# Optimization experiments

Measured on AMD Instinct MI355X. Metric: run time of the kernel, lower is better.

## Reference

```python
import jax, jax.numpy as jnp
import numpy as np
from jax.scipy.special import logsumexp, gammaln

B, T, D, K = 2048, 512, 64, 16  # num_sequences, max_length, data_dim (tones), hidden_dim per factor


def setup_inputs() -> dict:
    key = jax.random.key(0)
    k0, k1, k2, k3, k4 = jax.random.split(key, 5)
    sequences = jax.random.randint(k0, (B, T, D), 0, 2).astype(jnp.int32)  # binary piano-roll obs
    lengths = jax.random.randint(k1, (B,), 1, T + 1).astype(jnp.int32)
    probs_w = jax.nn.softmax(jax.random.normal(k2, (K, K), dtype=jnp.float32), axis=-1)  # row-stochastic
    probs_x = jax.nn.softmax(jax.random.normal(k3, (K, K), dtype=jnp.float32), axis=-1)
    probs_y = jax.random.uniform(k4, (K, K, D), dtype=jnp.float32) * 0.98 + 0.01  # in (0.01, 0.99)
    return {"sequences": sequences, "lengths": lengths,
            "probs_w": probs_w, "probs_x": probs_x, "probs_y": probs_y}


def _dirichlet_logpdf_rows(p, conc):
    # sum over rows of Dirichlet(conc_row).log_prob(p_row)
    return (((conc - 1.0) * jnp.log(p)).sum()
            + gammaln(conc.sum(-1)).sum() - gammaln(conc).sum())


def _log_joint(sequences, lengths, probs_w, probs_x, probs_y):
    dt = probs_y.dtype
    logTw = jnp.log(probs_w)            # (K, K) transition for w factor
    logTx = jnp.log(probs_x)            # (K, K) transition for x factor
    lp = jnp.log(probs_y)               # (K, K, D)
    l1p = jnp.log1p(-probs_y)           # (K, K, D)
    Wemit = (lp - l1p).reshape(K * K, D)        # Bernoulli log-odds per joint state
    base = l1p.sum(-1).reshape(K * K)           # sum_d log(1-p)

    ys = jnp.swapaxes(sequences, 0, 1)          # (T, B, D) int
    mask = jnp.arange(T)[:, None] < lengths[None, :]  # (T, B)

    # alpha[b, w, x]: forward log-prob; initial deterministic state (w, x) = (0, 0)
    alpha0 = jnp.full((B, K, K), -1e9, dtype=dt).at[:, 0, 0].set(0.0)

    def step(alpha, inp):
        y_t, m_t = inp
        y_f = y_t.astype(dt)                                    # (B, D)
        logE = (y_f @ Wemit.T + base).reshape(B, K, K)          # emission log-prob per (w', x')
        # marginalize previous w: (B, x, w')
        tmp = logsumexp(alpha[:, :, :, None] + logTw[None, :, None, :], axis=1)
        # marginalize previous x: (B, w', x')
        new = logsumexp(tmp[:, :, :, None] + logTx[None, :, None, :], axis=1)
        new = new + logE
        alpha = jnp.where(m_t[:, None, None], new, alpha)       # frozen past sequence end
        return alpha, None

    alpha, _ = jax.lax.scan(step, alpha0, (ys, mask))
    seq_ll = logsumexp(alpha.reshape(B, K * K), axis=-1)        # (B,) marginal log-likelihood

    # priors: Dirichlet(0.9*I + 0.1) on transition rows, Beta(0.1, 0.9) on probs_y
    conc = 0.9 * jnp.eye(K, dtype=dt) + 0.1
    prior = _dirichlet_logpdf_rows(probs_w, conc) + _dirichlet_logpdf_rows(probs_x, conc)
    a, b = 0.1, 0.9
    log_beta_norm = gammaln(a) + gammaln(b) - gammaln(a + b)
    prior = prior + ((a - 1.0) * lp + (b - 1.0) * l1p).sum() - log_beta_norm * (K * K * D)

    return seq_ll.sum() + prior


def reference(sequences, lengths, probs_w, probs_x, probs_y):
    return _log_joint(sequences, lengths, probs_w, probs_x, probs_y)
```

## Files before the change

### kernel.cpp

```cpp
#include <hip/hip_runtime.h>
#include <math.h>

#define NB 2048
#define NT 512
#define ND 64

typedef float    f32x4 __attribute__((ext_vector_type(4)));
typedef short    s16x8 __attribute__((ext_vector_type(8)));

#define MFMA32(A,B,C) __builtin_amdgcn_mfma_f32_16x16x32_bf16((A),(B),(C),0,0,0)

#if __has_builtin(__builtin_amdgcn_exp2f)
#define EXP2F(x) __builtin_amdgcn_exp2f(x)
#else
#define EXP2F(x) __expf((x) * 0.6931471805599453f)
#endif
#if __has_builtin(__builtin_amdgcn_logf)
#define LOG2F(x) __builtin_amdgcn_logf(x)
#else
#define LOG2F(x) (__logf(x) * 1.4426950408889634f)
#endif
#if __has_builtin(__builtin_amdgcn_rcpf)
#define RCPF(x) __builtin_amdgcn_rcpf(x)
#else
#define RCPF(x) __fdividef(1.0f, (x))
#endif

__device__ __forceinline__ unsigned short bf16rn(float f) {
  unsigned u = __float_as_uint(f);
  unsigned r = u + 0x7FFFu + ((u >> 16) & 1u);
  return (unsigned short)(r >> 16);
}
__device__ __forceinline__ unsigned pack2(float a, float b) {
  return (unsigned)bf16rn(a) | ((unsigned)bf16rn(b) << 16);
}
__device__ __forceinline__ unsigned pack2t(float a, float b) {
  return (__float_as_uint(a) >> 16) | (__float_as_uint(b) & 0xFFFF0000u);
}

union frag8 { s16x8 s8; unsigned u[4]; };

__device__ __forceinline__ s16x8 pack8t(f32x4 x) {
  frag8 r;
  r.u[0] = pack2t(x[0], x[1]);
  r.u[1] = pack2t(x[2], x[3]);
  r.u[2] = 0u; r.u[3] = 0u;
  return r.s8;
}

__global__ void fhmm_init_sort(const float* __restrict__ py,
                               const int* __restrict__ lengths,
                               unsigned short* __restrict__ ws16,
                               float* __restrict__ partials,
                               int* __restrict__ perm)
{
  const float LOG2E = 1.4426950408889634f;
  if (blockIdx.x == 12) {
    __shared__ int hist[512];
    __shared__ int cnt[512];
    __shared__ int sa[512], sb2[512];
    const int tid = threadIdx.x;
    hist[tid] = 0; hist[tid + 256] = 0;
    cnt[tid] = 0;  cnt[tid + 256] = 0;
    __syncthreads();
    int myb[8];
#pragma unroll
    for (int u = 0; u < 8; ++u) {
      int i = tid + 256 * u;
      myb[u] = 512 - lengths[i];
      atomicAdd(&hist[myb[u]], 1);
    }
    __syncthreads();
    sa[tid] = hist[tid]; sa[tid + 256] = hist[tid + 256];
    __syncthreads();
    int* src = sa; int* dst = sb2;
    for (int off = 1; off < 512; off <<= 1) {
      for (int k = tid; k < 512; k += 256)
        dst[k] = src[k] + ((k >= off) ? src[k - off] : 0);
      __syncthreads();
      int* tp = src; src = dst; dst = tp;
    }
#pragma unroll
    for (int u = 0; u < 8; ++u) {
      int i = tid + 256 * u;
      int b2 = myb[u];
      int pos = src[b2] - hist[b2] + atomicAdd(&cnt[b2], 1);
      perm[pos] = i;
    }
    return;
  }
  int t = blockIdx.x * 256 + threadIdx.x;
  if (t < 2048) partials[t] = 0.f;
  if (t < 2048) {
    int st = t >> 7, kk = (t >> 6) & 1, l = t & 63;
    int rho = st * 16 + (l & 15);
    int s = (4 * (rho >> 6) + (rho & 3)) * 16 + ((rho >> 2) & 15);
    int d0 = kk * 32 + 8 * (l >> 4);
    unsigned short* dst = ws16 + (size_t)t * 8;
#pragma unroll
    for (int i = 0; i < 8; ++i) {
      float p = py[s * 64 + d0 + i];
      dst[i] = bf16rn((logf(p) - log1pf(-p)) * LOG2E);
    }
  } else if (t < 3072) {
    int t2 = t - 2048;
    int st = t2 >> 6, l = t2 & 63;
    unsigned short v[8] = {0, 0, 0, 0, 0, 0, 0, 0};
    if (l < 16) {
      int rho = st * 16 + l;
      int s = (4 * (rho >> 6) + (rho & 3)) * 16 + ((rho >> 2) & 15);
      float base = 0.f;
      for (int d = 0; d < 64; ++d) base += log1pf(-py[s * 64 + d]);
      base *= LOG2E;
      unsigned short hi = bf16rn(base);
      float basehi = __uint_as_float(((unsigned)hi) << 16);
      v[0] = hi;
      v[1] = bf16rn(base - basehi);
    }
    unsigned short* dst = ws16 + (size_t)(2048 + t2) * 8;
#pragma unroll
    for (int i = 0; i < 8; ++i) dst[i] = v[i];
  }
}

__global__ __launch_bounds__(256, 2) void fhmm_fwd2(
    const int* __restrict__ seq, const int* __restrict__ lengths,
    const float* __restrict__ pw, const float* __restrict__ px,
    const void* __restrict__ wfrag, const int* __restrict__ perm,
    float* __restrict__ partials)
{
  __shared__ f32x4 e_lds[4][1024];

  const int tid = threadIdx.x;
  const int wv = tid >> 6, j = tid & 63;
  const int q = j >> 4, tl = j & 15;
  const int bid = blockIdx.x;
  const int lb  = (bid < 256) ? bid : (767 - bid);
  const int b = perm[(lb << 2) | wv];
  if (b < 0 || b >= NB) return;
  f32x4* e_w = e_lds[wv];
  const s16x8* wf_g = (const s16x8*)wfrag;
  const s16x8* w2_g = wf_g + 2048;

  s16x8 twb8, txb8;
  {
    frag8 a, c;
    a.u[0] = pack2(pw[(4 * q + 0) * 16 + tl], pw[(4 * q + 1) * 16 + tl]);
    a.u[1] = pack2(pw[(4 * q + 2) * 16 + tl], pw[(4 * q + 3) * 16 + tl]);
    a.u[2] = 0u; a.u[3] = 0u;
    c.u[0] = pack2(px[(4 * q + 0) * 16 + tl], px[(4 * q + 1) * 16 + tl]);
    c.u[1] = pack2(px[(4 * q + 2) * 16 + tl], px[(4 * q + 3) * 16 + tl]);
    c.u[2] = 0u; c.u[3] = 0u;
    twb8 = a.s8; txb8 = c.s8;
  }

  s16x8 f2 = {0, 0, 0, 0, 0, 0, 0, 0};
  if (q == 0) { f2[0] = (short)0x3F80; f2[1] = (short)0x3F80; }

  s16x8 ones8;
  {
    frag8 o;
    o.u[0] = 0x3F803F80u; o.u[1] = 0x3F803F80u;
    o.u[2] = 0x3F803F80u; o.u[3] = 0x3F803F80u;
    ones8 = o.s8;
  }

  f32x4 p = {0.f, 0.f, 0.f, 0.f};
  if (j == 0) p[0] = 1.f;

  const int len = lengths[b];
  const int* ybase = seq + (size_t)b * NT * ND;

  int4 ya0, ya1, yb0, yb1;
  {
    const int* yr = ybase + (size_t)tl * ND + 8 * q;
    const int4* pp  = (const int4*)yr;
    const int4* pp2 = (const int4*)(yr + 32);
    ya0 = pp[0]; ya1 = pp[1]; yb0 = pp2[0]; yb1 = pp2[1];
  }

  float L2 = 0.f, Ls = 0.f, R = 0.f;
  const f32x4 z4 = {0.f, 0.f, 0.f, 0.f};

  for (int t0 = 0; t0 < len; t0 += 16) {
    union { s16x8 s; unsigned u[4]; } f0u, f1u;
    f0u.u[0] = (ya0.x ? 0x3F80u : 0u) | (ya0.y ? 0x3F800000u : 0u);
    f0u.u[1] = (ya0.z ? 0x3F80u : 0u) | (ya0.w ? 0x3F800000u : 0u);
    f0u.u[2] = (ya1.x ? 0x3F80u : 0u) | (ya1.y ? 0x3F800000u : 0u);
    f0u.u[3] = (ya1.z ? 0x3F80u : 0u) | (ya1.w ? 0x3F800000u : 0u);
    f1u.u[0] = (yb0.x ? 0x3F80u : 0u) | (yb0.y ? 0x3F800000u : 0u);
    f1u.u[1] = (yb0.z ? 0x3F80u : 0u) | (yb0.w ? 0x3F800000u : 0u);
    f1u.u[2] = (yb1.x ? 0x3F80u : 0u) | (yb1.y ? 0x3F800000u : 0u);
    f1u.u[3] = (yb1.z ? 0x3F80u : 0u) | (yb1.w ? 0x3F800000u : 0u);
    const s16x8 f0 = f0u.s, f1 = f1u.s;

    if (t0 + 16 < len) {
      const int* yr = ybase + (size_t)(t0 + 16 + tl) * ND + 8 * q;
      const int4* pp  = (const int4*)yr;
      const int4* pp2 = (const int4*)(yr + 32);
      ya0 = pp[0]; ya1 = pp[1]; yb0 = pp2[0]; yb1 = pp2[1];
    }

#pragma unroll
    for (int st = 0; st < 16; ++st) {
      f32x4 acc = MFMA32(w2_g[st * 64 + j], f2, z4);
      acc = MFMA32(wf_g[(2 * st + 0) * 64 + j], f0, acc);
      acc = MFMA32(wf_g[(2 * st + 1) * 64 + j], f1, acc);
      f32x4 G;
      G[0] = EXP2F(fminf(acc[0] - R, 80.f));
      G[1] = EXP2F(fminf(acc[1] - R, 80.f));
      G[2] = EXP2F(fminf(acc[2] - R, 80.f));
      G[3] = EXP2F(fminf(acc[3] - R, 80.f));
      e_w[tl * 64 + ((st * 4 + q) ^ tl)] = G;
    }

    const int nsteps = (len - t0 < 16) ? (len - t0) : 16;
    float LsC = 0.f;
    f32x4 gv = e_w[j];
    for (int it = 0; it < nsteps; ++it) {
      const f32x4 g = gv;
      const int itn = (it + 1) & 15;
      gv = e_w[itn * 64 + (j ^ itn)];
      s16x8 vb = pack8t(p);
      f32x4 P  = MFMA32(vb, twb8, z4);
      f32x4 S1 = MFMA32(vb, ones8, z4);
      f32x4 U  = MFMA32(pack8t(P), txb8, z4);
      f32x4 S2 = MFMA32(pack8t(S1), ones8, z4);
      const float s   = fmaxf(S2[0], 1e-30f);
      const float inv = RCPF(s);
      LsC += LOG2F(s);
      f32x4 pn;
      pn[0] = (U[0] * inv) * g[0];
      pn[1] = (U[1] * inv) * g[1];
      pn[2] = (U[2] * inv) * g[2];
      pn[3] = (U[3] * inv) * g[3];
      p = pn;
    }
    L2 += (float)nsteps * R;
    Ls += LsC;
    R  += LsC * 0.0625f;
  }
  {
    f32x4 F1 = MFMA32(pack8t(p), ones8, z4);
    f32x4 F2 = MFMA32(pack8t(F1), ones8, z4);
    float sf = fmaxf(F2[0], 1e-35f);
    float L = (L2 + Ls + LOG2F(sf)) * 0.6931471805599453f;
    if (j == 0) partials[b] = L;
  }
}

__global__ __launch_bounds__(256, 3) void fhmm_fwd1(
    const int* __restrict__ seq, const int* __restrict__ lengths,
    const float* __restrict__ pw, const float* __restrict__ px,
    const float* __restrict__ py, float* __restrict__ partials,
    float* __restrict__ out)
{
  const int b = blockIdx.x, tid = threadIdx.x;
  const int wp = tid >> 4, xc = tid & 15;
  float Twc[16], Txc[16], W[64], base = 0.f;
#pragma unroll
  for (int w = 0; w < 16; ++w) Twc[w] = pw[w * 16 + wp];
#pragma unroll
  for (int x = 0; x < 16; ++x) Txc[x] = px[x * 16 + xc];
#pragma unroll
  for (int d = 0; d < 64; ++d) {
    float pv = py[tid * 64 + d];
    W[d] = logf(pv) - log1pf(-pv);
    base += log1pf(-pv);
  }
  __shared__ __align__(16) float yf[64];
  __shared__ __align__(16) float v_s[256];
  __shared__ __align__(16) float tmp_s[256];
  __shared__ float red[8];
  const int len = lengths[b];
  const int* yb = seq + (size_t)b * (NT * ND);
  v_s[tid] = (tid == 0) ? 1.f : 0.f;
  float L = 0.f, ynext = 0.f;
  if (tid < 64) ynext = (float)yb[tid];
  for (int t = 0; t < len; ++t) {
    if (tid < 64) yf[tid] = ynext;
    __syncthreads();
    if (tid < 64 && (t + 1) < len) ynext = (float)yb[(t + 1) * ND + tid];
    float e0 = base, e1 = 0.f, e2 = 0.f, e3 = 0.f;
    const float4* y4p = (const float4*)yf;
#pragma unroll
    for (int i = 0; i < 16; ++i) {
      float4 y4 = y4p[i];
      e0 = fmaf(y4.x, W[4 * i + 0], e0); e1 = fmaf(y4.y, W[4 * i + 1], e1);
      e2 = fmaf(y4.z, W[4 * i + 2], e2); e3 = fmaf(y4.w, W[4 * i + 3], e3);
    }
    float e = (e0 + e1) + (e2 + e3);
    float s1a = 0.f, s1b = 0.f;
#pragma unroll
    for (int w = 0; w < 16; w += 2) {
      s1a = fmaf(Twc[w], v_s[w * 16 + xc], s1a);
      s1b = fmaf(Twc[w + 1], v_s[(w + 1) * 16 + xc], s1b);
    }
    tmp_s[tid] = s1a + s1b;
    float mm = e;
#pragma unroll
    for (int off = 32; off; off >>= 1) mm = fmaxf(mm, __shfl_xor(mm, off));
    if ((tid & 63) == 0) red[tid >> 6] = mm;
    __syncthreads();
    mm = fmaxf(fmaxf(red[0], red[1]), fmaxf(red[2], red[3]));
    float q0 = 0.f, q1 = 0.f;
    const float4* t4p = (const float4*)(tmp_s + wp * 16);
#pragma unroll
    for (int i = 0; i < 4; ++i) {
      float4 t4 = t4p[i];
      q0 = fmaf(t4.x, Txc[4 * i + 0], q0); q1 = fmaf(t4.y, Txc[4 * i + 1], q1);
      q0 = fmaf(t4.z, Txc[4 * i + 2], q0); q1 = fmaf(t4.w, Txc[4 * i + 3], q1);
    }
    float val = (q0 + q1) * __expf(e - mm);
    float s = val;
#pragma unroll
    for (int off = 32; off; off >>= 1) s += __shfl_xor(s, off);
    if ((tid & 63) == 0) red[4 + (tid >> 6)] = s;
    __syncthreads();
    s = (red[4] + red[5]) + (red[6] + red[7]);
    L += __logf(s) + mm;
    v_s[tid] = val * (1.0f / s);
  }
  if (partials) { if (tid == 0) partials[b] = L; }
  else { if (tid == 0) atomicAdd(out, L); }
}

__global__ void fhmm_finalize(const float* __restrict__ partials,
                              const float* __restrict__ pw,
                              const float* __restrict__ px,
                              const float* __restrict__ py,
                              float* __restrict__ out)
{
  const int tid = threadIdx.x;
  float a = 0.f;
  if (partials) {
#pragma unroll
    for (int i = 0; i < 8; ++i) a += partials[tid + 256 * i];
  }
  {
    int i = tid >> 4, j = tid & 15;
    if (i != j) a += -0.9f * (logf(pw[tid]) + logf(px[tid]));
  }
  for (int k = 0; k < 64; ++k) {
    float p = py[tid * 64 + k];
    a += -0.9f * logf(p) - 0.1f * log1pf(-p);
  }
  __shared__ float red[256];
  red[tid] = a;
  __syncthreads();
  for (int s = 128; s > 0; s >>= 1) {
    if (tid < s) red[tid] += red[tid + s];
    __syncthreads();
  }
  if (tid == 0) {
    const float cst =
        2.f * (16.f * 0.2846828704729192f - 240.f * 2.2527126517342055f)
        - (2.2527126517342055f + 0.0663762397347443f) * 16384.f;
    out[0] = red[0] + cst;
  }
}

extern "C" void kernel_launch(void* const* d_in, const int* in_sizes, int n_in,
                              void* d_out, int out_size, void* d_ws, size_t ws_size,
                              hipStream_t stream) {
  const int*   seq = (const int*)d_in[0];
  const int*   len = (const int*)d_in[1];
  const float* pw  = (const float*)d_in[2];
  const float* px  = (const float*)d_in[3];
  const float* py  = (const float*)d_in[4];
  float*       out = (float*)d_out;

  const size_t NEED = 65536;
  if (ws_size >= NEED) {
    unsigned short* wf = (unsigned short*)d_ws;
    float* partials = (float*)((char*)d_ws + 49152);
    int*   perm     = (int*)((char*)d_ws + 57344);
    fhmm_init_sort<<<13, 256, 0, stream>>>(py, len, wf, partials, perm);
    fhmm_fwd2<<<512, 256, 0, stream>>>(seq, len, pw, px, (const void*)wf, perm, partials);
    fhmm_finalize<<<1, 256, 0, stream>>>(partials, pw, px, py, out);
  } else if (ws_size >= 2048 * sizeof(float)) {
    float* partials = (float*)d_ws;
    fhmm_fwd1<<<NB, 256, 0, stream>>>(seq, len, pw, px, py, partials, out);
    fhmm_finalize<<<1, 256, 0, stream>>>(partials, pw, px, py, out);
  } else {
    fhmm_finalize<<<1, 256, 0, stream>>>(nullptr, pw, px, py, out);
    fhmm_fwd1<<<NB, 256, 0, stream>>>(seq, len, pw, px, py, nullptr, out);
  }
}
```

Measured before the change: 200.8 us.

## Split each sequence into parallel forward and backward halves meeting at midpoint

Adds a new kernel in which each sequence is handled by two waves: one runs the scaled forward recursion over the first half and the other runs a backward recursion from the end down to the midpoint. A separate combine kernel takes the dot product of the alpha and beta vectors to recover each sequence's log-likelihood. The aim is to halve the serial dependency chain per sequence and double the number of active waves, with emission values stored in LDS as bf16 to cut shared-memory use. The cost is an extra kernel launch, global traffic for the intermediate vectors, a larger workspace requirement, and lower precision in the stored emissions.

```diff
diff --git a/kernel.cpp b/kernel.cpp
--- a/kernel.cpp
+++ b/kernel.cpp
@@ -123,6 +123,196 @@
   }
 }
 
+__global__ __launch_bounds__(256, 4) void fhmm_fwd3(
+    const int* __restrict__ seq, const int* __restrict__ lengths,
+    const float* __restrict__ pw, const float* __restrict__ px,
+    const void* __restrict__ wfrag, const int* __restrict__ perm,
+    float* __restrict__ alphaM, float* __restrict__ betaM,
+    float* __restrict__ scal)
+{
+  __shared__ uint2 e_lds[4][1024];
+
+  const int tid = threadIdx.x;
+  const int wv = tid >> 6, j = tid & 63;
+  const int q = j >> 4, tl = j & 15;
+  const int bid = blockIdx.x;
+  const int lb  = (bid < 512) ? bid : (1535 - bid);
+  const int rank = 2 * lb + (wv >> 1);
+  const int h = wv & 1;
+  const int b = perm[rank];
+  if (b < 0 || b >= NB) return;
+  uint2* e_w = e_lds[wv];
+  const s16x8* wf_g = (const s16x8*)wfrag;
+  const s16x8* w2_g = wf_g + 2048;
+
+  s16x8 twb8, txb8;
+  {
+    frag8 a, c;
+    if (h == 0) {
+      a.u[0] = pack2(pw[(4 * q + 0) * 16 + tl], pw[(4 * q + 1) * 16 + tl]);
+      a.u[1] = pack2(pw[(4 * q + 2) * 16 + tl], pw[(4 * q + 3) * 16 + tl]);
+      c.u[0] = pack2(px[(4 * q + 0) * 16 + tl], px[(4 * q + 1) * 16 + tl]);
+      c.u[1] = pack2(px[(4 * q + 2) * 16 + tl], px[(4 * q + 3) * 16 + tl]);
+    } else {
+      a.u[0] = pack2(pw[tl * 16 + 4 * q + 0], pw[tl * 16 + 4 * q + 1]);
+      a.u[1] = pack2(pw[tl * 16 + 4 * q + 2], pw[tl * 16 + 4 * q + 3]);
+      c.u[0] = pack2(px[tl * 16 + 4 * q + 0], px[tl * 16 + 4 * q + 1]);
+      c.u[1] = pack2(px[tl * 16 + 4 * q + 2], px[tl * 16 + 4 * q + 3]);
+    }
+    a.u[2] = 0u; a.u[3] = 0u; c.u[2] = 0u; c.u[3] = 0u;
+    twb8 = a.s8; txb8 = c.s8;
+  }
+
+  s16x8 f2 = {0, 0, 0, 0, 0, 0, 0, 0};
+  if (q == 0) { f2[0] = (short)0x3F80; f2[1] = (short)0x3F80; }
+
+  s16x8 ones8;
+  {
+    frag8 o;
+    o.u[0] = 0x3F803F80u; o.u[1] = 0x3F803F80u;
+    o.u[2] = 0x3F803F80u; o.u[3] = 0x3F803F80u;
+    ones8 = o.s8;
+  }
+
+  const int len = lengths[b];
+  const int mid = len >> 1;
+  const int* ybase = seq + (size_t)b * NT * ND;
+  const f32x4 z4 = {0.f, 0.f, 0.f, 0.f};
+
+  f32x4 p;
+  if (h == 0) { p = z4; if (j == 0) p[0] = 1.f; }
+  else { p[0] = 1.f; p[1] = 1.f; p[2] = 1.f; p[3] = 1.f; }
+
+  float L2 = 0.f, Ls = 0.f, R = 0.f;
+
+  for (int k = 0;; ++k) {
+    int t_lo, ns;
+    if (h == 0) {
+      t_lo = 16 * k;
+      if (t_lo >= mid) break;
+      ns = mid - t_lo; if (ns > 16) ns = 16;
+    } else {
+      int t_hi = len - 16 * k;
+      if (t_hi <= mid) break;
+      t_lo = t_hi - 16; if (t_lo < mid) t_lo = mid;
+      ns = t_hi - t_lo;
+    }
+
+    s16x8 f0, f1;
+    {
+      int row = t_lo + tl;
+      if (row > len - 1) row = len - 1;
+      const int* yr = ybase + (size_t)row * ND + 8 * q;
+      const int4 ya0 = ((const int4*)yr)[0];
+      const int4 ya1 = ((const int4*)yr)[1];
+      const int4 yb0 = ((const int4*)(yr + 32))[0];
+      const int4 yb1 = ((const int4*)(yr + 32))[1];
+      frag8 f0u, f1u;
+      f0u.u[0] = (ya0.x ? 0x3F80u : 0u) | (ya0.y ? 0x3F800000u : 0u);
+      f0u.u[1] = (ya0.z ? 0x3F80u : 0u) | (ya0.w ? 0x3F800000u : 0u);
+      f0u.u[2] = (ya1.x ? 0x3F80u : 0u) | (ya1.y ? 0x3F800000u : 0u);
+      f0u.u[3] = (ya1.z ? 0x3F80u : 0u) | (ya1.w ? 0x3F800000u : 0u);
+      f1u.u[0] = (yb0.x ? 0x3F80u : 0u) | (yb0.y ? 0x3F800000u : 0u);
+      f1u.u[1] = (yb0.z ? 0x3F80u : 0u) | (yb0.w ? 0x3F800000u : 0u);
+      f1u.u[2] = (yb1.x ? 0x3F80u : 0u) | (yb1.y ? 0x3F800000u : 0u);
+      f1u.u[3] = (yb1.z ? 0x3F80u : 0u) | (yb1.w ? 0x3F800000u : 0u);
+      f0 = f0u.s8; f1 = f1u.s8;
+    }
+
+#pragma unroll
+    for (int st = 0; st < 16; ++st) {
+      f32x4 acc = MFMA32(w2_g[st * 64 + j], f2, z4);
+      acc = MFMA32(wf_g[(2 * st + 0) * 64 + j], f0, acc);
+      acc = MFMA32(wf_g[(2 * st + 1) * 64 + j], f1, acc);
+      float G0 = EXP2F(fminf(acc[0] - R, 80.f));
+      float G1 = EXP2F(fminf(acc[1] - R, 80.f));
+      float G2 = EXP2F(fminf(acc[2] - R, 80.f));
+      float G3 = EXP2F(fminf(acc[3] - R, 80.f));
+      e_w[tl * 64 + ((st * 4 + q) ^ tl)] = make_uint2(pack2t(G0, G1), pack2t(G2, G3));
+    }
+
+    float LsC = 0.f;
+    if (h == 0) {
+      uint2 ev = e_w[j];
+      for (int it = 0; it < ns; ++it) {
+        const uint2 ec = ev;
+        const int itn = (it + 1) & 15;
+        ev = e_w[itn * 64 + (j ^ itn)];
+        f32x4 g;
+        g[0] = __uint_as_float(ec.x << 16);
+        g[1] = __uint_as_float(ec.x & 0xFFFF0000u);
+        g[2] = __uint_as_float(ec.y << 16);
+        g[3] = __uint_as_float(ec.y & 0xFFFF0000u);
+        s16x8 vb = pack8t(p);
+        f32x4 P  = MFMA32(vb, twb8, z4);
+        f32x4 S1 = MFMA32(vb, ones8, z4);
+        f32x4 U  = MFMA32(pack8t(P), txb8, z4);
+        f32x4 S2 = MFMA32(pack8t(S1), ones8, z4);
+        const float s   = fmaxf(S2[0], 1e-30f);
+        const float inv = RCPF(s);
+        LsC += LOG2F(s);
+        p[0] = (U[0] * inv) * g[0];
+        p[1] = (U[1] * inv) * g[1];
+        p[2] = (U[2] * inv) * g[2];
+        p[3] = (U[3] * inv) * g[3];
+      }
+    } else {
+      int it0 = ns - 1;
+      uint2 ev = e_w[it0 * 64 + (j ^ it0)];
+      for (int it = it0; it >= 0; --it) {
+        const uint2 ec = ev;
+        const int itn = (it - 1) & 15;
+        ev = e_w[itn * 64 + (j ^ itn)];
+        f32x4 u4;
+        u4[0] = p[0] * __uint_as_float(ec.x << 16);
+        u4[1] = p[1] * __uint_as_float(ec.x & 0xFFFF0000u);
+        u4[2] = p[2] * __uint_as_float(ec.y << 16);
+        u4[3] = p[3] * __uint_as_float(ec.y & 0xFFFF0000u);
+        s16x8 vb = pack8t(u4);
+        f32x4 P  = MFMA32(vb, twb8, z4);
+        f32x4 S1 = MFMA32(vb, ones8, z4);
+        f32x4 U  = MFMA32(pack8t(P), txb8, z4);
+        f32x4 S2 = MFMA32(pack8t(S1), ones8, z4);
+        const float s   = fmaxf(S2[0], 1e-30f);
+        const float inv = RCPF(s);
+        LsC += LOG2F(s);
+        p[0] = U[0] * inv;
+        p[1] = U[1] * inv;
+        p[2] = U[2] * inv;
+        p[3] = U[3] * inv;
+      }
+    }
+    L2 += (float)ns * R;
+    Ls += LsC;
+    R  += LsC * 0.0625f;
+  }
+
+  {
+    float* outv = (h ? betaM : alphaM) + (size_t)b * 256 + j * 4;
+    *(f32x4*)outv = p;
+    if (j == 0) scal[2 * b + h] = L2 + Ls;
+  }
+}
+
+__global__ void fhmm_combine(const float* __restrict__ alphaM,
+                             const float* __restrict__ betaM,
+                             const float* __restrict__ scal,
+                             float* __restrict__ partials)
+{
+  const int b = blockIdx.x, tid = threadIdx.x;
+  float v = alphaM[(size_t)b * 256 + tid] * betaM[(size_t)b * 256 + tid];
+#pragma unroll
+  for (int off = 1; off < 64; off <<= 1) v += __shfl_xor(v, off);
+  __shared__ float red[4];
+  if ((tid & 63) == 0) red[tid >> 6] = v;
+  __syncthreads();
+  if (tid == 0) {
+    float dot = fmaxf((red[0] + red[1]) + (red[2] + red[3]), 1e-35f);
+    partials[b] = (scal[2 * b] + scal[2 * b + 1] + LOG2F(dot))
+                  * 0.6931471805599453f;
+  }
+}
+
 __global__ __launch_bounds__(256, 2) void fhmm_fwd2(
     const int* __restrict__ seq, const int* __restrict__ lengths,
     const float* __restrict__ pw, const float* __restrict__ px,
@@ -174,16 +364,15 @@
   int4 ya0, ya1, yb0, yb1;
   {
     const int* yr = ybase + (size_t)tl * ND + 8 * q;
-    const int4* pp  = (const int4*)yr;
-    const int4* pp2 = (const int4*)(yr + 32);
-    ya0 = pp[0]; ya1 = pp[1]; yb0 = pp2[0]; yb1 = pp2[1];
+    ya0 = ((const int4*)yr)[0]; ya1 = ((const int4*)yr)[1];
+    yb0 = ((const int4*)(yr + 32))[0]; yb1 = ((const int4*)(yr + 32))[1];
   }
 
   float L2 = 0.f, Ls = 0.f, R = 0.f;
   const f32x4 z4 = {0.f, 0.f, 0.f, 0.f};
 
   for (int t0 = 0; t0 < len; t0 += 16) {
-    union { s16x8 s; unsigned u[4]; } f0u, f1u;
+    frag8 f0u, f1u;
     f0u.u[0] = (ya0.x ? 0x3F80u : 0u) | (ya0.y ? 0x3F800000u : 0u);
     f0u.u[1] = (ya0.z ? 0x3F80u : 0u) | (ya0.w ? 0x3F800000u : 0u);
     f0u.u[2] = (ya1.x ? 0x3F80u : 0u) | (ya1.y ? 0x3F800000u : 0u);
@@ -192,13 +381,12 @@
     f1u.u[1] = (yb0.z ? 0x3F80u : 0u) | (yb0.w ? 0x3F800000u : 0u);
     f1u.u[2] = (yb1.x ? 0x3F80u : 0u) | (yb1.y ? 0x3F800000u : 0u);
     f1u.u[3] = (yb1.z ? 0x3F80u : 0u) | (yb1.w ? 0x3F800000u : 0u);
-    const s16x8 f0 = f0u.s, f1 = f1u.s;
+    const s16x8 f0 = f0u.s8, f1 = f1u.s8;
 
     if (t0 + 16 < len) {
       const int* yr = ybase + (size_t)(t0 + 16 + tl) * ND + 8 * q;
-      const int4* pp  = (const int4*)yr;
-      const int4* pp2 = (const int4*)(yr + 32);
-      ya0 = pp[0]; ya1 = pp[1]; yb0 = pp2[0]; yb1 = pp2[1];
+      ya0 = ((const int4*)yr)[0]; ya1 = ((const int4*)yr)[1];
+      yb0 = ((const int4*)(yr + 32))[0]; yb1 = ((const int4*)(yr + 32))[1];
     }
 
 #pragma unroll
@@ -370,15 +558,28 @@
   const float* py  = (const float*)d_in[4];
   float*       out = (float*)d_out;
 
-  const size_t NEED = 65536;
-  if (ws_size >= NEED) {
+  const size_t NEED1 = 65536;
+  const size_t NEED2 = NEED1 + (size_t)2 * NB * 256 * 4 + NB * 2 * 4;
+  if (ws_size >= NEED2) {
+    unsigned short* wf = (unsigned short*)d_ws;
+    float* partials = (float*)((char*)d_ws + 49152);
+    int*   perm     = (int*)((char*)d_ws + 57344);
+    float* alphaM   = (float*)((char*)d_ws + 65536);
+    float* betaM    = alphaM + (size_t)NB * 256;
+    float* scal     = betaM + (size_t)NB * 256;
+    fhmm_init_sort<<<13, 256, 0, stream>>>(py, len, wf, partials, perm);
+    fhmm_fwd3<<<1024, 256, 0, stream>>>(seq, len, pw, px, (const void*)wf,
+                                        perm, alphaM, betaM, scal);
+    fhmm_combine<<<NB, 256, 0, stream>>>(alphaM, betaM, scal, partials);
+    fhmm_finalize<<<1, 256, 0, stream>>>(partials, pw, px, py, out);
+  } else if (ws_size >= NEED1) {
     unsigned short* wf = (unsigned short*)d_ws;
     float* partials = (float*)((char*)d_ws + 49152);
     int*   perm     = (int*)((char*)d_ws + 57344);
     fhmm_init_sort<<<13, 256, 0, stream>>>(py, len, wf, partials, perm);
     fhmm_fwd2<<<512, 256, 0, stream>>>(seq, len, pw, px, (const void*)wf, perm, partials);
     fhmm_finalize<<<1, 256, 0, stream>>>(partials, pw, px, py, out);
-  } else if (ws_size >= 2048 * sizeof(float)) {
+  } else if (ws_size >= NB * sizeof(float)) {
     float* partials = (float*)d_ws;
     fhmm_fwd1<<<NB, 256, 0, stream>>>(seq, len, pw, px, py, partials, out);
     fhmm_finalize<<<1, 256, 0, stream>>>(partials, pw, px, py, out);
```

After: 211.3 us. 5.2% more time.
